# Performance work log

Measured on AMD Instinct MI355X. Metric: run time of the kernel, lower is better.

## Reference

```python
import jax, jax.numpy as jnp
import numpy as np

B = 4096
N = 8192
LEVEL_SIZES = [8, 128, 2048, 6008]  # sums to N; 4-level taxonomy
EPS = 1e-07


def _build_hierarchy():
    """parent[c] = parent node index (-1 for roots); level_of[c] = depth."""
    rng = np.random.default_rng(0)
    parent = np.full(N, -1, np.int32)
    level_of = np.zeros(N, np.int32)
    off, prev_start, prev_size = 0, 0, 0
    for l, sz in enumerate(LEVEL_SIZES):
        level_of[off:off + sz] = l
        if l > 0:
            parent[off:off + sz] = rng.integers(prev_start, prev_start + prev_size, sz)
        prev_start, prev_size = off, sz
        off += sz
    return parent, level_of


def setup_inputs() -> dict:
    key = jax.random.key(0)
    k1, k2 = jax.random.split(key)
    pred = jax.random.normal(k1, (B, N), dtype=jnp.float32)  # logits
    target = (jax.random.uniform(k2, (B, N)) < 0.02).astype(jnp.float32)
    parent_np, level_np = _build_hierarchy()
    return {
        "pred": pred,
        "target": target,
        "parent": jnp.asarray(parent_np),
        "level_of": jnp.asarray(level_np),
        "mode": 0,  # 0 = EVAL (propagate conditional probs), 1 = TRAIN
    }


def reference(pred, target, parent, level_of, mode):
    p = jax.nn.sigmoid(pred)                      # [B, N]
    parent_clip = jnp.maximum(parent, 0)          # safe gather index for roots
    is_root = parent < 0                          # recursive_relation[-1]

    if mode != 1:  # not 'TRAIN': top-down conditional probability propagation
        pc = p
        for l in range(1, len(LEVEL_SIZES)):
            # pred_clone[:, children(n)] = pred[:, children] * pred_clone[:, n]
            pc = jnp.where(level_of == l, p * pc[:, parent_clip], pc)
        pred_clone = pc
    else:
        pred_clone = None

    # mask[b, c] = 1 if c is a root, or if target[b, parent[c]] == 1
    mask = jnp.where(is_root, jnp.float32(1.0), target[:, parent_clip])

    pcl = jnp.clip(p, EPS, 1.0 - EPS)
    loss = -(jnp.log(pcl) * target + (1.0 - target) * mask * jnp.log(1.0 - pcl))
    loss = loss.sum(axis=1).mean()
    return (loss, pred_clone)
```

## Files before the change

kernel.cpp:

```cpp
#include <hip/hip_runtime.h>


#define N_NODES 8192
#define L1S 8
#define L2S 136
#define L3S 2184
#define N4   (N_NODES / 4)
#define L3S4 (L3S / 4)

__device__ __forceinline__ float frcp(float x) { return __builtin_amdgcn_rcpf(x); }

__global__ __launch_bounds__(256) void cs_main(
    const float* __restrict__ pred,
    const float* __restrict__ target,
    const int* __restrict__ parent,
    float* __restrict__ out,
    float* __restrict__ bsum,
    float inv_b)
{
    __shared__ float2 pt[L3S];
    __shared__ float red[4];

    const int tid = threadIdx.x;
    const int b = blockIdx.x;
    const float* __restrict__ prow = pred + (size_t)b * N_NODES;
    const float* __restrict__ trow = target + (size_t)b * N_NODES;
    float* __restrict__ orow = out + 1 + (size_t)b * N_NODES;

    float lsum = 0.0f;

    for (int c4 = tid; c4 < L3S4; c4 += 256) {
        const int c0 = c4 * 4;
        const float4 x4 = ((const float4*)prow)[c4];
        const float4 t4 = ((const float4*)trow)[c4];
        const int4  q4 = ((const int4*)parent)[c4];
        const float xs[4] = {x4.x, x4.y, x4.z, x4.w};
        const float ts[4] = {t4.x, t4.y, t4.z, t4.w};
        const int   qs[4] = {q4.x, q4.y, q4.z, q4.w};
#pragma unroll
        for (int j = 0; j < 4; ++j) {
            const float x = xs[j], t = ts[j];
            const float e = __expf(-x);
            const float p = frcp(1.0f + e);
            const float s = __logf(1.0f + e);
            const float mask = (qs[j] < 0) ? 1.0f : trow[qs[j]];
            lsum += t * s + (1.0f - t) * mask * (s + x);
            pt[c0 + j] = make_float2(p, t);
        }
    }
    __syncthreads();

    for (int c = L1S + tid; c < L2S; c += 256) pt[c].x *= pt[parent[c]].x;
    __syncthreads();

    for (int c = tid; c < L3S; c += 256) {
        if (c < L2S) {
            orow[c] = pt[c].x;
        } else {
            const float v = pt[c].x * pt[parent[c]].x;
            pt[c].x = v;
            orow[c] = v;
        }
    }
    __syncthreads();

    int c4 = L3S4 + tid;
    float4 x4, t4; int4 q4;
    if (c4 < N4) {
        x4 = ((const float4*)prow)[c4];
        t4 = ((const float4*)trow)[c4];
        q4 = ((const int4*)parent)[c4];
    }
    while (c4 < N4) {
        const int n4 = c4 + 256;
        float4 nx, nt; int4 nq;
        if (n4 < N4) {
            nx = ((const float4*)prow)[n4];
            nt = ((const float4*)trow)[n4];
            nq = ((const int4*)parent)[n4];
        }
        const int c0 = c4 * 4;
        const float xs[4] = {x4.x, x4.y, x4.z, x4.w};
        const float ts[4] = {t4.x, t4.y, t4.z, t4.w};
        const int   qs[4] = {q4.x, q4.y, q4.z, q4.w};
#pragma unroll
        for (int j = 0; j < 4; ++j) {
            const float x = xs[j], t = ts[j];
            const float2 pm = pt[qs[j]];
            const float e = __expf(-x);
            const float p = frcp(1.0f + e);
            const float s = __logf(1.0f + e);
            lsum += t * s + (1.0f - t) * pm.y * (s + x);
            orow[c0 + j] = p * pm.x;
        }
        x4 = nx; t4 = nt; q4 = nq; c4 = n4;
    }

#pragma unroll
    for (int off = 32; off > 0; off >>= 1) lsum += __shfl_down(lsum, off);
    if ((tid & 63) == 0) red[tid >> 6] = lsum;
    __syncthreads();
    if (tid == 0) {
        const float s = (red[0] + red[1]) + (red[2] + red[3]);
        if (bsum) bsum[blockIdx.x] = s;
        else atomicAdd(out, s * inv_b);
    }
}

__global__ __launch_bounds__(256) void cs_finish(
    const float* __restrict__ bsum, float* __restrict__ out,
    int nblocks, float inv_b)
{
    __shared__ float red[4];
    const int tid = threadIdx.x;
    float s = 0.0f;
    for (int i = tid; i < nblocks; i += 256) s += bsum[i];
#pragma unroll
    for (int off = 32; off > 0; off >>= 1) s += __shfl_down(s, off);
    if ((tid & 63) == 0) red[tid >> 6] = s;
    __syncthreads();
    if (tid == 0) out[0] = ((red[0] + red[1]) + (red[2] + red[3])) * inv_b;
}

extern "C" void kernel_launch(void* const* d_in, const int* in_sizes, int n_in,
                              void* d_out, int out_size, void* d_ws, size_t ws_size,
                              hipStream_t stream) {
    const float* pred   = (const float*)d_in[0];
    const float* target = (const float*)d_in[1];
    const int*   parent = (const int*)d_in[2];

    float* out = (float*)d_out;
    const int batch = in_sizes[0] / N_NODES;
    const float inv_b = 1.0f / (float)batch;

    if (ws_size >= (size_t)batch * sizeof(float)) {
        float* bsum = (float*)d_ws;
        cs_main<<<batch, 256, 0, stream>>>(pred, target, parent, out, bsum, inv_b);
        cs_finish<<<1, 256, 0, stream>>>(bsum, out, batch, inv_b);
    } else {
        hipMemsetAsync(d_out, 0, sizeof(float), stream);
        cs_main<<<batch, 256, 0, stream>>>(pred, target, parent, out, nullptr, inv_b);
    }
}
```

Before: 92.94 us.

## Pack target bit into sign of shared prob, merge propagation levels

Stores a single float per node in shared memory, with the target encoded in the sign of the sigmoid probability, which halves LDS footprint and traffic. Levels 1 and 2 are computed in one pass using a grandparent lookup, which removes one barrier and the global target gather for the mask. The level-3 loop now loads two groups per iteration and writes output in aligned pieces (scalar, float2, scalar) because the output row starts one float past the base. The first levels now compute loss with two logs per element, and any row element whose target is exactly 0 but whose probability is 0 would read as untargeted.

```diff
diff --git a/kernel.cpp b/kernel.cpp
--- a/kernel.cpp
+++ b/kernel.cpp
@@ -18,7 +18,7 @@
     float* __restrict__ bsum,
     float inv_b)
 {
-    __shared__ float2 pt[L3S];
+    __shared__ float pk[L3S];
     __shared__ float red[4];
 
     const int tid = threadIdx.x;
@@ -30,70 +30,79 @@
     float lsum = 0.0f;
 
     for (int c4 = tid; c4 < L3S4; c4 += 256) {
-        const int c0 = c4 * 4;
         const float4 x4 = ((const float4*)prow)[c4];
         const float4 t4 = ((const float4*)trow)[c4];
-        const int4  q4 = ((const int4*)parent)[c4];
         const float xs[4] = {x4.x, x4.y, x4.z, x4.w};
         const float ts[4] = {t4.x, t4.y, t4.z, t4.w};
-        const int   qs[4] = {q4.x, q4.y, q4.z, q4.w};
+        const int c0 = c4 * 4;
 #pragma unroll
         for (int j = 0; j < 4; ++j) {
-            const float x = xs[j], t = ts[j];
-            const float e = __expf(-x);
-            const float p = frcp(1.0f + e);
-            const float s = __logf(1.0f + e);
-            const float mask = (qs[j] < 0) ? 1.0f : trow[qs[j]];
-            lsum += t * s + (1.0f - t) * mask * (s + x);
-            pt[c0 + j] = make_float2(p, t);
+            const float p = frcp(1.0f + __expf(-xs[j]));
+            pk[c0 + j] = ts[j] > 0.5f ? -p : p;
         }
     }
     __syncthreads();
 
-    for (int c = L1S + tid; c < L2S; c += 256) pt[c].x *= pt[parent[c]].x;
-    __syncthreads();
-
     for (int c = tid; c < L3S; c += 256) {
-        if (c < L2S) {
-            orow[c] = pt[c].x;
+        const float v = pk[c];
+        const float p = fabsf(v);
+        const float t = (v < 0.0f) ? 1.0f : 0.0f;
+        float mask, cum;
+        if (c < L1S) {
+            mask = 1.0f; cum = p;
+        } else if (c < L2S) {
+            const float pv = pk[parent[c]];
+            mask = (pv < 0.0f) ? 1.0f : 0.0f;
+            cum = p * fabsf(pv);
         } else {
-            const float v = pt[c].x * pt[parent[c]].x;
-            pt[c].x = v;
-            orow[c] = v;
+            const int pa = parent[c];
+            const float pv = pk[pa];
+            const float gv = pk[parent[pa]];
+            mask = (pv < 0.0f) ? 1.0f : 0.0f;
+            cum = p * fabsf(pv) * fabsf(gv);
+            pk[c] = (t > 0.0f) ? -cum : cum;
         }
+        lsum += t * (-__logf(p)) + (1.0f - t) * mask * (-__logf(1.0f - p));
+        orow[c] = cum;
     }
     __syncthreads();
 
-    int c4 = L3S4 + tid;
-    float4 x4, t4; int4 q4;
-    if (c4 < N4) {
-        x4 = ((const float4*)prow)[c4];
-        t4 = ((const float4*)trow)[c4];
-        q4 = ((const int4*)parent)[c4];
-    }
-    while (c4 < N4) {
-        const int n4 = c4 + 256;
-        float4 nx, nt; int4 nq;
-        if (n4 < N4) {
-            nx = ((const float4*)prow)[n4];
-            nt = ((const float4*)trow)[n4];
-            nq = ((const int4*)parent)[n4];
-        }
-        const int c0 = c4 * 4;
+    auto proc = [&](int g, const float4& x4, const float4& t4, const int4& q4) {
         const float xs[4] = {x4.x, x4.y, x4.z, x4.w};
         const float ts[4] = {t4.x, t4.y, t4.z, t4.w};
         const int   qs[4] = {q4.x, q4.y, q4.z, q4.w};
+        float r[4];
 #pragma unroll
         for (int j = 0; j < 4; ++j) {
             const float x = xs[j], t = ts[j];
-            const float2 pm = pt[qs[j]];
+            const float pv = pk[qs[j]];
+            const float mask = (pv < 0.0f) ? 1.0f : 0.0f;
             const float e = __expf(-x);
+            const float s = __logf(1.0f + e);
             const float p = frcp(1.0f + e);
-            const float s = __logf(1.0f + e);
-            lsum += t * s + (1.0f - t) * pm.y * (s + x);
-            orow[c0 + j] = p * pm.x;
+            lsum += t * s + (1.0f - t) * mask * (s + x);
+            r[j] = p * fabsf(pv);
         }
-        x4 = nx; t4 = nt; q4 = nq; c4 = n4;
+        const int c0 = g * 4;
+        orow[c0] = r[0];
+        *(float2*)(orow + c0 + 1) = make_float2(r[1], r[2]);
+        orow[c0 + 3] = r[3];
+    };
+
+    for (int g0 = L3S4 + tid; g0 < N4; g0 += 512) {
+        const int g1 = g0 + 256;
+        const float4 xa = ((const float4*)prow)[g0];
+        const float4 ta = ((const float4*)trow)[g0];
+        const int4  qa = ((const int4*)parent)[g0];
+        const bool hb = (g1 < N4);
+        float4 xb, tb; int4 qb;
+        if (hb) {
+            xb = ((const float4*)prow)[g1];
+            tb = ((const float4*)trow)[g1];
+            qb = ((const int4*)parent)[g1];
+        }
+        proc(g0, xa, ta, qa);
+        if (hb) proc(g1, xb, tb, qb);
     }
 
 #pragma unroll
```

Result: no change. 92.10 us (-0.9%).
